# Kernel optimization log

Hardware: AMD Instinct MI355X
Metric: run time of the kernel (lower is better)

Reference implementation:

```python
import jax, jax.numpy as jnp
import numpy as np

C = 128  # in_channels

def setup_inputs() -> dict:
    key = jax.random.key(0)
    k1, k2, k3, k4 = jax.random.split(key, 4)
    b, c, h, w = 4, C, 64, 64
    feature0 = jax.random.normal(k1, (b, c, h, w), dtype=jnp.float32)
    flow = jax.random.normal(k2, (b, 2, h, w), dtype=jnp.float32)
    # Linear weights stored torch-style as [out, in]; xavier-uniform-like scale
    lim = float(np.sqrt(6.0 / (c + c)))
    Wq = jax.random.uniform(k3, (c, c), minval=-lim, maxval=lim, dtype=jnp.float32)
    Wk = jax.random.uniform(k4, (c, c), minval=-lim, maxval=lim, dtype=jnp.float32)
    bq = jnp.zeros((c,), dtype=jnp.float32)
    bk = jnp.zeros((c,), dtype=jnp.float32)
    return {"feature0": feature0, "flow": flow, "Wq": Wq, "bq": bq, "Wk": Wk, "bk": bk}

def reference(feature0, flow, Wq, bq, Wk, bk):
    b, c, h, w = feature0.shape
    n = h * w
    # [b, n, c]
    x = feature0.reshape(b, c, n).transpose(0, 2, 1)
    query = x @ Wq.T + bq                     # q_proj(feature0)
    key = query @ Wk.T + bk                   # NOTE: k_proj applied to query (as in source)
    value = flow.reshape(b, flow.shape[1], n).transpose(0, 2, 1)  # [b, n, 2]
    scores = jnp.einsum('bnc,bmc->bnm', query, key) / jnp.sqrt(jnp.float32(c))
    prob = jax.nn.softmax(scores, axis=-1)    # [b, n, n]
    out = jnp.einsum('bnm,bmv->bnv', prob, value)  # [b, n, 2]
    return out.reshape(b, h, w, value.shape[-1]).transpose(0, 3, 1, 2)
```

## Files before the change

kernel.cpp:

```cpp
#include <hip/hip_runtime.h>
#include <hip/hip_bf16.h>

constexpr int CH = 128;
constexpr int NPOS = 4096;
constexpr int NB = 4;
constexpr int SPLITS = 8;

typedef __bf16 bf16x8 __attribute__((ext_vector_type(8)));
typedef float f32x2 __attribute__((ext_vector_type(2)));
typedef float f32x16 __attribute__((ext_vector_type(16)));

constexpr float CSC = 0.08838834764831845f * 1.4426950408889634f;


__device__ __forceinline__ void async_copy16(const void* g, void* l) {
  auto gp = (const __attribute__((address_space(1))) unsigned int*)((uintptr_t)g);
  auto lp = (__attribute__((address_space(3))) unsigned int*)((uintptr_t)l);
  __builtin_amdgcn_global_load_lds(gp, lp, 16, 0, 0);
}

#define PIPE_BARRIER(N)                                              \
  asm volatile("s_waitcnt vmcnt(" #N ") lgkmcnt(0)\n\ts_barrier" ::: "memory")

__global__ __launch_bounds__(128) void fuse_w_kernel(
    const float* __restrict__ Wq, const float* __restrict__ bq,
    const float* __restrict__ Wk, const float* __restrict__ bk,
    __bf16* __restrict__ Wqb, __bf16* __restrict__ Wqkb,
    float* __restrict__ bqk) {
  __shared__ float red[CH];
  const int o = blockIdx.x;
  const int i = threadIdx.x;
  float acc = 0.f;
#pragma unroll 8
  for (int m = 0; m < CH; m++) acc += Wk[o * CH + m] * Wq[m * CH + i];
  Wqkb[o * CH + i] = (__bf16)acc;
  Wqb[o * CH + i] = (__bf16)Wq[o * CH + i];
  red[i] = Wk[o * CH + i] * bq[i];
  __syncthreads();
  if (i == 0) {
    float s = 0.f;
    for (int m = 0; m < CH; m++) s += red[m];
    bqk[o] = s + bk[o];
  }
}

__global__ __launch_bounds__(512) void proj_kernel(
    const float* __restrict__ feature0, const __bf16* __restrict__ Wqb,
    const float* __restrict__ bq, const __bf16* __restrict__ Wqkb,
    const float* __restrict__ bqk, __bf16* __restrict__ Qf,
    __bf16* __restrict__ Kf) {
  __shared__ __bf16 Alds[8 * 512];

  const int bid = blockIdx.x;
  const int b = (bid >> 1) & 3;
  const int u = (bid >> 3) * 2 + (bid & 1);
  const int tid = threadIdx.x;
  const int lane = tid & 63;
  const int half = lane >> 5, l31 = lane & 31;
  const int wv = tid >> 6;
  const int z = wv >> 2, n = wv & 3;

  {
    const int p = tid & 31;
    const int c0 = tid >> 5;
    const float* src = feature0 + (size_t)(b * CH) * NPOS + u * 32 + p;
#pragma unroll
    for (int r = 0; r < 8; r++) {
      const int c = r * 16 + c0;
      const float v = src[(size_t)c * NPOS];
      const int ks = c >> 4, hf = (c >> 3) & 1, j = c & 7;
      Alds[ks * 512 + (p + 32 * hf) * 8 + j] = (__bf16)v;
    }
  }
  __syncthreads();

  bf16x8 A[8];
#pragma unroll
  for (int ks = 0; ks < 8; ks++)
    A[ks] = *(const bf16x8*)(&Alds[ks * 512 + lane * 8]);

  const __bf16* W = z ? Wqkb : Wqb;
  const float* bias = z ? bqk : bq;
  __bf16* Out = z ? Kf : Qf;
  const float scale = z ? 1.0f : CSC;

  const int co = n * 32 + l31;
  const bf16x8* Bp = (const bf16x8*)(W + co * CH + half * 8);
  f32x16 c = {0.f, 0.f, 0.f, 0.f, 0.f, 0.f, 0.f, 0.f,
              0.f, 0.f, 0.f, 0.f, 0.f, 0.f, 0.f, 0.f};
#pragma unroll
  for (int ks = 0; ks < 8; ks++)
    c = __builtin_amdgcn_mfma_f32_32x32x16_bf16(A[ks], Bp[ks * 2], c, 0, 0, 0);
  const float bv = bias[co];
  const int kf = n * 2 + (l31 >> 4);
  const int lanebit = (l31 >> 3) & 1;
  const int j = l31 & 7;
#pragma unroll
  for (int r = 0; r < 16; r++) {
    int roff = (r & 3) + 8 * (r >> 2) + 4 * half;
    Out[((((size_t)(b * (NPOS / 32) + u)) * 8 + kf) * 64 +
         (roff + 32 * lanebit)) * 8 + j] = (__bf16)((c[r] + bv) * scale);
  }
}

__global__ __launch_bounds__(512, 2) void attn_kernel(
    const __bf16* __restrict__ Qf, const __bf16* __restrict__ Kf,
    const float* __restrict__ flow, float* __restrict__ part) {
  __shared__ __bf16 Klds[3][8 * 512];
  __shared__ float flds[2 * 512];
  __shared__ float red[256 * 3];

  const int bid = blockIdx.x;
  const int b = (bid >> 1) & 3;
  const int u = (bid >> 3) * 2 + (bid & 1);
  const int split = u >> 4;
  const int qg = u & 15;

  const int tid = threadIdx.x;
  const int wave = tid >> 6, lane = tid & 63;
  const int half = lane >> 5, l31 = lane & 31;
  const int kbase = split * (NPOS / SPLITS);
  constexpr int NT = NPOS / SPLITS / 32;

  {
    const float* fl0 = flow + (size_t)(b * 2 + 0) * NPOS + kbase;
    const float* fl1 = flow + (size_t)(b * 2 + 1) * NPOS + kbase;
    flds[tid] = fl0[tid];
    flds[512 + tid] = fl1[tid];
  }

  const int qt = qg * 8 + wave;
  bf16x8 qf[8];
  {
    const bf16x8* Qp =
        (const bf16x8*)Qf + ((size_t)(b * (NPOS / 32) + qt) * 8) * 64 + lane;
#pragma unroll
    for (int kf = 0; kf < 8; kf++) qf[kf] = Qp[kf * 64];
  }

  const __bf16* Ktb = Kf + ((size_t)(b * (NPOS / 32) + (kbase >> 5))) * 4096;

  auto issue = [&](int t, int buf) {
    const __bf16* g = Ktb + (size_t)t * 4096;
    async_copy16(g + wave * 512 + lane * 8,
                 &Klds[buf][wave * 512 + lane * 8]);
  };
  issue(0, 0);
  issue(1, 1);

  float ls[16];
  f32x2 av[16];
#pragma unroll
  for (int r = 0; r < 16; r++) {
    ls[r] = 0.f;
    av[r] = f32x2{0.f, 0.f};
  }

  int bcur = 0, bnext = 2;
  for (int t = 0; t < NT; t++) {
    PIPE_BARRIER(1);
    if (t + 2 < NT) issue(t + 2, bnext);

    const __bf16* kb = &Klds[bcur][0];
    f32x16 c = {0.f, 0.f, 0.f, 0.f, 0.f, 0.f, 0.f, 0.f,
                0.f, 0.f, 0.f, 0.f, 0.f, 0.f, 0.f, 0.f};
#pragma unroll
    for (int kf = 0; kf < 8; kf++) {
      bf16x8 bfrag = *(const bf16x8*)(kb + kf * 512 + lane * 8);
      c = __builtin_amdgcn_mfma_f32_32x32x16_bf16(qf[kf], bfrag, c, 0, 0, 0);
    }
    const f32x2 v01 = {flds[t * 32 + l31], flds[512 + t * 32 + l31]};
#pragma unroll
    for (int r = 0; r < 16; r++) {
      float p = __builtin_amdgcn_exp2f(c[r]);
      ls[r] += p;
      av[r] += f32x2{p, p} * v01;
    }
    bcur = (bcur == 2) ? 0 : bcur + 1;
    bnext = (bnext == 2) ? 0 : bnext + 1;
  }

#pragma unroll
  for (int r = 0; r < 16; r++) {
#pragma unroll
    for (int st = 1; st < 32; st <<= 1) {
      ls[r] += __shfl_xor(ls[r], st, 64);
      av[r][0] += __shfl_xor(av[r][0], st, 64);
      av[r][1] += __shfl_xor(av[r][1], st, 64);
    }
  }
  if (l31 == 0) {
#pragma unroll
    for (int r = 0; r < 16; r++) {
      int ql = wave * 32 + (r & 3) + 8 * (r >> 2) + 4 * half;
      red[ql * 3 + 0] = ls[r];
      red[ql * 3 + 1] = av[r][0];
      red[ql * 3 + 2] = av[r][1];
    }
  }
  __syncthreads();
  for (int idx = tid; idx < 256 * 3; idx += 512) {
    int plane = idx >> 8, ql = idx & 255;
    part[((size_t)(plane * SPLITS + split) * NB + b) * NPOS + qg * 256 + ql] =
        red[ql * 3 + plane];
  }
}

__global__ __launch_bounds__(256) void combine_kernel(
    const float* __restrict__ part, float* __restrict__ out) {
  int t = blockIdx.x * 256 + threadIdx.x;
  int b = t >> 12, q = t & (NPOS - 1);
  float l = 0.f, x = 0.f, y = 0.f;
#pragma unroll
  for (int s = 0; s < SPLITS; s++) {
    l += part[((size_t)(0 * SPLITS + s) * NB + b) * NPOS + q];
    x += part[((size_t)(1 * SPLITS + s) * NB + b) * NPOS + q];
    y += part[((size_t)(2 * SPLITS + s) * NB + b) * NPOS + q];
  }
  float inv = 1.0f / l;
  out[(size_t)(b * 2 + 0) * NPOS + q] = x * inv;
  out[(size_t)(b * 2 + 1) * NPOS + q] = y * inv;
}

extern "C" void kernel_launch(void* const* d_in, const int* in_sizes, int n_in,
                              void* d_out, int out_size, void* d_ws,
                              size_t ws_size, hipStream_t stream) {
  const float* feature0 = (const float*)d_in[0];
  const float* flow = (const float*)d_in[1];
  const float* Wq = (const float*)d_in[2];
  const float* bq = (const float*)d_in[3];
  const float* Wk = (const float*)d_in[4];
  const float* bk = (const float*)d_in[5];
  float* out = (float*)d_out;

  char* ws = (char*)d_ws;
  __bf16* Qf = (__bf16*)ws;
  __bf16* Kf = (__bf16*)(ws + (4 << 20));
  __bf16* Wqb = (__bf16*)(ws + (8 << 20));
  __bf16* Wqkb = (__bf16*)(ws + (8 << 20) + (32 << 10));
  float* bqk = (float*)(ws + (8 << 20) + (64 << 10));
  float* part = (float*)(ws + (8 << 20) + (128 << 10));

  fuse_w_kernel<<<dim3(CH), 128, 0, stream>>>(Wq, bq, Wk, bk, Wqb, Wqkb, bqk);
  proj_kernel<<<dim3(512), 512, 0, stream>>>(feature0, Wqb, bq, Wqkb, bqk, Qf,
                                             Kf);
  attn_kernel<<<dim3(512), 512, 0, stream>>>(Qf, Kf, flow, part);
  combine_kernel<<<dim3(NB * NPOS / 256), 256, 0, stream>>>(part, out);
}
```

Baseline: 113.8 us.

## Compute two query tiles per wave in attention to reuse K fragments

The attention kernel drops to 256 threads per block, and each wave now handles two 32-row query tiles instead of one. Each K fragment read from LDS feeds two MFMAs, which halves LDS reads per MFMA and gives the scheduler independent MFMA chains to interleave. Each wave now issues two async copies per K tile, so the pipeline wait count becomes 2, with a full drain on the last iteration. The cost is twice the accumulator and softmax-state registers per wave, plus fewer waves per block to hide latency.

```diff
diff --git a/kernel.cpp b/kernel.cpp
--- a/kernel.cpp
+++ b/kernel.cpp
@@ -103,7 +103,7 @@
   }
 }
 
-__global__ __launch_bounds__(512, 2) void attn_kernel(
+__global__ __launch_bounds__(256, 2) void attn_kernel(
     const __bf16* __restrict__ Qf, const __bf16* __restrict__ Kf,
     const float* __restrict__ flow, float* __restrict__ part) {
   __shared__ __bf16 Klds[3][8 * 512];
@@ -126,55 +126,73 @@
     const float* fl0 = flow + (size_t)(b * 2 + 0) * NPOS + kbase;
     const float* fl1 = flow + (size_t)(b * 2 + 1) * NPOS + kbase;
     flds[tid] = fl0[tid];
+    flds[256 + tid] = fl0[256 + tid];
     flds[512 + tid] = fl1[tid];
-  }
-
-  const int qt = qg * 8 + wave;
-  bf16x8 qf[8];
+    flds[768 + tid] = fl1[256 + tid];
+  }
+
+  const int qt0 = qg * 8 + wave * 2;
+  bf16x8 qf0[8], qf1[8];
   {
     const bf16x8* Qp =
-        (const bf16x8*)Qf + ((size_t)(b * (NPOS / 32) + qt) * 8) * 64 + lane;
-#pragma unroll
-    for (int kf = 0; kf < 8; kf++) qf[kf] = Qp[kf * 64];
+        (const bf16x8*)Qf + ((size_t)(b * (NPOS / 32) + qt0) * 8) * 64 + lane;
+#pragma unroll
+    for (int kf = 0; kf < 8; kf++) {
+      qf0[kf] = Qp[kf * 64];
+      qf1[kf] = Qp[512 + kf * 64];
+    }
   }
 
   const __bf16* Ktb = Kf + ((size_t)(b * (NPOS / 32) + (kbase >> 5))) * 4096;
 
   auto issue = [&](int t, int buf) {
     const __bf16* g = Ktb + (size_t)t * 4096;
-    async_copy16(g + wave * 512 + lane * 8,
-                 &Klds[buf][wave * 512 + lane * 8]);
+    const int c0 = wave * 1024;
+    async_copy16(g + c0 + lane * 8, &Klds[buf][c0 + lane * 8]);
+    async_copy16(g + c0 + 512 + lane * 8, &Klds[buf][c0 + 512 + lane * 8]);
   };
   issue(0, 0);
   issue(1, 1);
 
-  float ls[16];
-  f32x2 av[16];
+  float ls0[16], ls1[16];
+  f32x2 av0[16], av1[16];
 #pragma unroll
   for (int r = 0; r < 16; r++) {
-    ls[r] = 0.f;
-    av[r] = f32x2{0.f, 0.f};
+    ls0[r] = 0.f;
+    ls1[r] = 0.f;
+    av0[r] = f32x2{0.f, 0.f};
+    av1[r] = f32x2{0.f, 0.f};
   }
 
   int bcur = 0, bnext = 2;
   for (int t = 0; t < NT; t++) {
-    PIPE_BARRIER(1);
+    if (t < NT - 1) {
+      PIPE_BARRIER(2);
+    } else {
+      PIPE_BARRIER(0);
+    }
     if (t + 2 < NT) issue(t + 2, bnext);
 
     const __bf16* kb = &Klds[bcur][0];
-    f32x16 c = {0.f, 0.f, 0.f, 0.f, 0.f, 0.f, 0.f, 0.f,
-                0.f, 0.f, 0.f, 0.f, 0.f, 0.f, 0.f, 0.f};
+    f32x16 c0 = {0.f, 0.f, 0.f, 0.f, 0.f, 0.f, 0.f, 0.f,
+                 0.f, 0.f, 0.f, 0.f, 0.f, 0.f, 0.f, 0.f};
+    f32x16 c1 = {0.f, 0.f, 0.f, 0.f, 0.f, 0.f, 0.f, 0.f,
+                 0.f, 0.f, 0.f, 0.f, 0.f, 0.f, 0.f, 0.f};
 #pragma unroll
     for (int kf = 0; kf < 8; kf++) {
       bf16x8 bfrag = *(const bf16x8*)(kb + kf * 512 + lane * 8);
-      c = __builtin_amdgcn_mfma_f32_32x32x16_bf16(qf[kf], bfrag, c, 0, 0, 0);
+      c0 = __builtin_amdgcn_mfma_f32_32x32x16_bf16(qf0[kf], bfrag, c0, 0, 0, 0);
+      c1 = __builtin_amdgcn_mfma_f32_32x32x16_bf16(qf1[kf], bfrag, c1, 0, 0, 0);
     }
     const f32x2 v01 = {flds[t * 32 + l31], flds[512 + t * 32 + l31]};
 #pragma unroll
     for (int r = 0; r < 16; r++) {
-      float p = __builtin_amdgcn_exp2f(c[r]);
-      ls[r] += p;
-      av[r] += f32x2{p, p} * v01;
+      float p0 = __builtin_amdgcn_exp2f(c0[r]);
+      ls0[r] += p0;
+      av0[r] += f32x2{p0, p0} * v01;
+      float p1 = __builtin_amdgcn_exp2f(c1[r]);
+      ls1[r] += p1;
+      av1[r] += f32x2{p1, p1} * v01;
     }
     bcur = (bcur == 2) ? 0 : bcur + 1;
     bnext = (bnext == 2) ? 0 : bnext + 1;
@@ -184,22 +202,30 @@
   for (int r = 0; r < 16; r++) {
 #pragma unroll
     for (int st = 1; st < 32; st <<= 1) {
-      ls[r] += __shfl_xor(ls[r], st, 64);
-      av[r][0] += __shfl_xor(av[r][0], st, 64);
-      av[r][1] += __shfl_xor(av[r][1], st, 64);
+      ls0[r] += __shfl_xor(ls0[r], st, 64);
+      av0[r][0] += __shfl_xor(av0[r][0], st, 64);
+      av0[r][1] += __shfl_xor(av0[r][1], st, 64);
+      ls1[r] += __shfl_xor(ls1[r], st, 64);
+      av1[r][0] += __shfl_xor(av1[r][0], st, 64);
+      av1[r][1] += __shfl_xor(av1[r][1], st, 64);
     }
   }
   if (l31 == 0) {
 #pragma unroll
     for (int r = 0; r < 16; r++) {
-      int ql = wave * 32 + (r & 3) + 8 * (r >> 2) + 4 * half;
-      red[ql * 3 + 0] = ls[r];
-      red[ql * 3 + 1] = av[r][0];
-      red[ql * 3 + 2] = av[r][1];
+      int roff = (r & 3) + 8 * (r >> 2) + 4 * half;
+      int ql0 = (wave * 2 + 0) * 32 + roff;
+      int ql1 = (wave * 2 + 1) * 32 + roff;
+      red[ql0 * 3 + 0] = ls0[r];
+      red[ql0 * 3 + 1] = av0[r][0];
+      red[ql0 * 3 + 2] = av0[r][1];
+      red[ql1 * 3 + 0] = ls1[r];
+      red[ql1 * 3 + 1] = av1[r][0];
+      red[ql1 * 3 + 2] = av1[r][1];
     }
   }
   __syncthreads();
-  for (int idx = tid; idx < 256 * 3; idx += 512) {
+  for (int idx = tid; idx < 256 * 3; idx += 256) {
     int plane = idx >> 8, ql = idx & 255;
     part[((size_t)(plane * SPLITS + split) * NB + b) * NPOS + qg * 256 + ql] =
         red[ql * 3 + plane];
@@ -244,6 +270,6 @@
   fuse_w_kernel<<<dim3(CH), 128, 0, stream>>>(Wq, bq, Wk, bk, Wqb, Wqkb, bqk);
   proj_kernel<<<dim3(512), 512, 0, stream>>>(feature0, Wqb, bq, Wqkb, bqk, Qf,
                                              Kf);
-  attn_kernel<<<dim3(512), 512, 0, stream>>>(Qf, Kf, flow, part);
+  attn_kernel<<<dim3(512), 256, 0, stream>>>(Qf, Kf, flow, part);
   combine_kernel<<<dim3(NB * NPOS / 256), 256, 0, stream>>>(part, out);
 }
```

Measured after the change: 113.8 us. No clear change (-0.0%).
